# Kernel tuning notes

Measured on AMD Instinct MI355X. Metric: run time of the kernel, lower is better.

## Reference

```python
import jax, jax.numpy as jnp
import numpy as np

EPS = 1e-5
C = 512


def conv1x1(x, w, b):
    # 1x1 conv == per-pixel linear: x [B,C,H,W], w [O,C], b [O]
    return jnp.einsum('bchw,oc->bohw', x, w) + b[None, :, None, None]


def mean_variance_norm(feat):
    # per (batch, channel) normalization over spatial dims, unbiased var + eps
    b, c, h, w = feat.shape
    flat = feat.reshape(b, c, h * w)
    mean = flat.mean(axis=2)[:, :, None, None]
    std = jnp.sqrt(jnp.var(flat, axis=2, ddof=1) + EPS)[:, :, None, None]
    return (feat - mean) / std


def setup_inputs() -> dict:
    key = jax.random.key(0)
    ks = jax.random.split(key, 10)
    sc = 1.0 / np.sqrt(C)
    inp = {
        'content': jax.random.normal(ks[0], (2, C, 64, 64), jnp.float32),
        'style': jax.random.normal(ks[1], (2, C, 64, 64), jnp.float32),
        'f_w': jax.random.normal(ks[2], (C, C), jnp.float32) * sc,
        'f_b': jnp.zeros((C,), jnp.float32),
        'g_w': jax.random.normal(ks[3], (C, C), jnp.float32) * sc,
        'g_b': jnp.zeros((C,), jnp.float32),
        'h_w': jax.random.normal(ks[4], (C, C), jnp.float32) * sc,
        'h_b': jnp.zeros((C,), jnp.float32),
        'out_w': jax.random.normal(ks[5], (C, C), jnp.float32) * sc,
        'out_b': jnp.zeros((C,), jnp.float32),
    }
    return inp


def reference(content, style, f_w, f_b, g_w, g_b, h_w, h_b, out_w, out_b):
    b, c, h, w = content.shape
    Fq = conv1x1(content, f_w, f_b).reshape(b, c, h * w).transpose(0, 2, 1)  # [b,Nc,C]
    Gk = conv1x1(style, g_w, g_b).reshape(b, c, -1)                           # [b,C,Ns]
    Hv = conv1x1(style, h_w, h_b).reshape(b, c, -1).transpose(0, 2, 1)        # [b,Ns,C]

    S = jax.nn.softmax(jnp.einsum('bnc,bcs->bns', Fq, Gk), axis=-1)           # [b,Nc,Ns]
    mean = jnp.einsum('bns,bsc->bnc', S, Hv)                                   # E[x]
    second = jnp.einsum('bns,bsc->bnc', S, Hv * Hv)                            # E[x^2]
    std = jnp.sqrt(jnp.maximum(second - mean * mean, 0.0))

    mean = mean.reshape(b, h, w, c).transpose(0, 3, 1, 2)
    std = std.reshape(b, h, w, c).transpose(0, 3, 1, 2)

    O = std * mean_variance_norm(content) + mean
    O = conv1x1(O, out_w, out_b)
    return O + content
```

## Files before the change

### kernel.cpp

```cpp
#include <hip/hip_runtime.h>
#include <math.h>

#define NS 4096
#define CH 512
#define EPSV 1e-5f

typedef __attribute__((ext_vector_type(8))) _Float16 f16x8;
typedef __attribute__((ext_vector_type(4))) float f32x4;
typedef unsigned short u16;

__device__ __forceinline__ u16 f2h(float x) {
    _Float16 h = (_Float16)x;
    return __builtin_bit_cast(unsigned short, h);
}
__device__ __forceinline__ float h2f(u16 b) {
    return (float)__builtin_bit_cast(_Float16, b);
}

__device__ __forceinline__ void gload16(const void* g, void* l) {
    __builtin_amdgcn_global_load_lds((const __attribute__((address_space(1))) unsigned*)g,
                                     (__attribute__((address_space(3))) unsigned*)l, 16, 0, 0);
}

struct ZTab {
    long aoff[6];
    long boff[6];
    long ooff[6];
    long coff[6];
    int  mode[6];
    int  np[6];
    const float* bias[6];
};

template<int NPZ, bool GS>
__device__ __forceinline__ void kloop(
    const u16* __restrict__ pAhi, const u16* __restrict__ pAlo,
    const u16* __restrict__ pBhi,
    u16* smem, int smemStride,
    int Mw, int Nw, int K, int m0, int n0,
    int wid, int lane, int lk, int lm, int wm, int wn,
    const float* __restrict__ cbase,
    f32x4 (&acc)[4][4])
{
    auto stage = [&](int buf, int ks) {
        const int kp0 = ks << 2;
        #pragma unroll
        for (int i = 0; i < 2 * NPZ; ++i) {
            const int q = i * 4 + wid;
            const int b = q >> 3;
            const int p = (q & 7) >> 1;
            const int w = ((q & 1) << 6) + lane;
            const u16* src;
            if (b == 0)      src = pAhi + ((size_t)(kp0 + p) * Mw + m0 + w) * 8;
            else if (b == 1) src = pBhi + ((size_t)(kp0 + p) * Nw + n0 + w) * 8;
            else             src = pAlo + ((size_t)(kp0 + p) * Mw + m0 + w) * 8;
            gload16(src, &smem[(size_t)buf * smemStride + (size_t)(((b * 4 + p) * 128) + w) * 8]);
        }
    };

    const int nK = K >> 5;
    stage(0, 0);
    __syncthreads();
    int cur = 0;
    _Float16 ch[4] = {};
    for (int ks = 0; ks < nK; ++ks) {
        if (GS && (ks & 3) == 0) {
            const int g = ks >> 2;
            #pragma unroll
            for (int j = 0; j < 4; ++j)
                ch[j] = (_Float16)cbase[(size_t)g * NS + n0 + wn * 64 + j * 16 + lm];
        }
        if (ks + 1 < nK) stage(cur ^ 1, ks + 1);
        const u16* sm = smem + (size_t)cur * smemStride;
        f16x8 ah[4], bh[4], al[4];
        #pragma unroll
        for (int f = 0; f < 4; ++f) {
            ah[f] = *(const f16x8*)&sm[((0 * 4 + lk) * 128 + wm * 64 + f * 16 + lm) * 8];
            bh[f] = *(const f16x8*)&sm[((1 * 4 + lk) * 128 + wn * 64 + f * 16 + lm) * 8];
            if (GS) bh[f] = bh[f] * ch[f];
            if (NPZ == 3)
                al[f] = *(const f16x8*)&sm[((2 * 4 + lk) * 128 + wm * 64 + f * 16 + lm) * 8];
        }
        #pragma unroll
        for (int i = 0; i < 4; ++i)
            #pragma unroll
            for (int j = 0; j < 4; ++j) {
                acc[i][j] = __builtin_amdgcn_mfma_f32_16x16x32_f16(ah[i], bh[j], acc[i][j], 0, 0, 0);
                if (NPZ == 3)
                    acc[i][j] = __builtin_amdgcn_mfma_f32_16x16x32_f16(al[i], bh[j], acc[i][j], 0, 0, 0);
            }
        __syncthreads();
        cur ^= 1;
    }
}

template<int NP, bool RESID, bool COLST, bool GS>
__global__ __launch_bounds__(256, (NP == 2 ? 4 : 3)) void gemm_split(
    const u16* __restrict__ Ahi, const u16* __restrict__ Alo,
    const u16* __restrict__ Bhi,
    const float* __restrict__ resid,
    float* __restrict__ outF, u16* __restrict__ outH,
    float* __restrict__ pmg, float* __restrict__ psg,
    const float* __restrict__ cb,
    int Mw, int Nw, int K, ZTab tab)
{
    __shared__ u16 smem[2][NP * 4 * 128 * 8];
    const int t = threadIdx.x;
    const int lane = t & 63;
    const int wid = t >> 6;
    const int wm = wid >> 1, wn = wid & 1;
    const int lk = lane >> 4, lm = lane & 15;
    const int m0 = blockIdx.y * 128, n0 = blockIdx.x * 128;
    const int z = blockIdx.z;
    const int npz = tab.np[z];
    const u16* pAhi = Ahi + tab.aoff[z];
    const u16* pAlo = Alo + tab.aoff[z];
    const u16* pBhi = Bhi + tab.boff[z];
    const float* cbase = GS ? (cb + tab.coff[z]) : nullptr;

    f32x4 acc[4][4] = {};
    const int smemStride = NP * 4 * 128 * 8;

    if constexpr (NP == 2) {
        kloop<2, GS>(pAhi, pAlo, pBhi, &smem[0][0], smemStride,
                     Mw, Nw, K, m0, n0, wid, lane, lk, lm, wm, wn, cbase, acc);
    } else {
        if (npz == 2)
            kloop<2, GS>(pAhi, pAlo, pBhi, &smem[0][0], smemStride,
                         Mw, Nw, K, m0, n0, wid, lane, lk, lm, wm, wn, cbase, acc);
        else
            kloop<3, GS>(pAhi, pAlo, pBhi, &smem[0][0], smemStride,
                         Mw, Nw, K, m0, n0, wid, lane, lk, lm, wm, wn, cbase, acc);
    }

    const float* bp = tab.bias[z];
    if (COLST) {
        float* smx = (float*)&smem[0][0];
        float* ssm = smx + 256;
        #pragma unroll
        for (int j = 0; j < 4; ++j) {
            float mx = -3.0e38f;
            #pragma unroll
            for (int i = 0; i < 4; ++i)
                #pragma unroll
                for (int r = 0; r < 4; ++r)
                    mx = fmaxf(mx, acc[i][j][r]);
            mx = fmaxf(mx, __shfl_xor(mx, 16));
            mx = fmaxf(mx, __shfl_xor(mx, 32));
            float sum = 0.f;
            #pragma unroll
            for (int i = 0; i < 4; ++i)
                #pragma unroll
                for (int r = 0; r < 4; ++r)
                    sum += __expf(acc[i][j][r] - mx);
            sum += __shfl_xor(sum, 16);
            sum += __shfl_xor(sum, 32);
            if (lk == 0) {
                const int nloc = wn * 64 + j * 16 + lm;
                smx[wm * 128 + nloc] = mx;
                ssm[wm * 128 + nloc] = sum;
            }
        }
        __syncthreads();
        float mxc[4];
        #pragma unroll
        for (int j = 0; j < 4; ++j) {
            const int nloc = wn * 64 + j * 16 + lm;
            const float m0v = smx[nloc], m1v = smx[128 + nloc];
            const float mc = fmaxf(m0v, m1v);
            mxc[j] = mc;
            if (wm == 0 && lk == 0) {
                const float sc = ssm[nloc] * __expf(m0v - mc) + ssm[128 + nloc] * __expf(m1v - mc);
                const int n = n0 + nloc;
                const size_t gi = ((size_t)z * 32 + (m0 >> 7)) * NS + n;
                pmg[gi] = mc;
                psg[gi] = sc;
            }
        }
        u16* ph = outH + tab.ooff[z];
        #pragma unroll
        for (int i = 0; i < 4; ++i) {
            const long rg = (long)((m0 + wm * 64) >> 3) + i * 2 + (lk >> 1);
            const int sub = (lk & 1) * 4;
            #pragma unroll
            for (int j = 0; j < 4; ++j) {
                const int n = n0 + wn * 64 + j * 16 + lm;
                const long idx = (rg * Nw + n) * 8 + sub;
                u16 h[4];
                #pragma unroll
                for (int r = 0; r < 4; ++r)
                    h[r] = f2h(__expf(acc[i][j][r] - mxc[j]));
                *(ushort4*)&ph[idx] = make_ushort4(h[0], h[1], h[2], h[3]);
            }
        }
    } else if (tab.mode[z] == 0) {
        float* pout = outF + tab.ooff[z];
        #pragma unroll
        for (int i = 0; i < 4; ++i) {
            #pragma unroll
            for (int r = 0; r < 4; ++r) {
                const int m = m0 + wm * 64 + i * 16 + lk * 4 + r;
                const float bv = bp ? bp[m] : 0.f;
                const size_t ro = (size_t)m * Nw + n0 + wn * 64 + lm;
                #pragma unroll
                for (int j = 0; j < 4; ++j) {
                    float v = acc[i][j][r] + bv;
                    if (RESID) v += resid[tab.ooff[z] + ro + j * 16];
                    pout[ro + j * 16] = v;
                }
            }
        }
    } else {
        u16* ph = outH + tab.ooff[z];
        #pragma unroll
        for (int i = 0; i < 4; ++i) {
            float bv[4];
            #pragma unroll
            for (int r = 0; r < 4; ++r) {
                const int m = m0 + wm * 64 + i * 16 + lk * 4 + r;
                bv[r] = bp ? bp[m] : 0.f;
            }
            const long rg = (long)((m0 + wm * 64) >> 3) + i * 2 + (lk >> 1);
            const int sub = (lk & 1) * 4;
            #pragma unroll
            for (int j = 0; j < 4; ++j) {
                const int n = n0 + wn * 64 + j * 16 + lm;
                const long idx = (rg * Nw + n) * 8 + sub;
                u16 h[4];
                #pragma unroll
                for (int r = 0; r < 4; ++r)
                    h[r] = f2h(acc[i][j][r] + bv[r]);
                *(ushort4*)&ph[idx] = make_ushort4(h[0], h[1], h[2], h[3]);
            }
        }
    }
}

__global__ __launch_bounds__(256) void packB_k(const float* __restrict__ X,
    u16* __restrict__ Hi, int Nw, long xB, long pB)
{
    const int n = blockIdx.x * 256 + threadIdx.x;
    const int p = blockIdx.y;
    const int z = blockIdx.z;
    const float* Xp = X + (size_t)z * xB + ((size_t)p * 8) * Nw + n;
    u16 hi[8];
    #pragma unroll
    for (int j = 0; j < 8; ++j)
        hi[j] = f2h(Xp[(size_t)j * Nw]);
    const size_t o = (size_t)z * pB + ((size_t)p * Nw + n) * 8;
    *(uint4*)&Hi[o] = *(const uint4*)hi;
}

__global__ __launch_bounds__(256) void packA_T(const float* __restrict__ W,
    u16* __restrict__ Hi, int Kdim)
{
    __shared__ float tile[64][65];
    const int t = threadIdx.x;
    const int k0 = blockIdx.x * 64, m0 = blockIdx.y * 64;
    const int kk = t & 63, mb = t >> 6;
    #pragma unroll
    for (int it = 0; it < 16; ++it) {
        int mm = mb + it * 4;
        tile[mm][kk] = W[(size_t)(m0 + mm) * Kdim + k0 + kk];
    }
    __syncthreads();
    #pragma unroll
    for (int cc = 0; cc < 2; ++cc) {
        int c = t + cc * 256;
        int kp = c >> 6, m = c & 63;
        u16 hi[8];
        #pragma unroll
        for (int j = 0; j < 8; ++j)
            hi[j] = f2h(tile[m][kp * 8 + j]);
        size_t o = ((size_t)(k0 / 8 + kp) * CH + m0 + m) * 8;
        *(uint4*)&Hi[o] = *(const uint4*)hi;
    }
}

__global__ __launch_bounds__(256) void pack_hvT(const float* __restrict__ Hv,
    u16* __restrict__ H1h, u16* __restrict__ H2h, u16* __restrict__ H2l)
{
    __shared__ float tile[64][65];
    const int t = threadIdx.x;
    const int s0 = blockIdx.x * 64, c0 = blockIdx.y * 64;
    const int z = blockIdx.z;
    const float* src = Hv + (size_t)z * CH * NS;
    const int ss = t & 63, cb = t >> 6;
    #pragma unroll
    for (int it = 0; it < 16; ++it) {
        int cc = cb + it * 4;
        tile[cc][ss] = src[(size_t)(c0 + cc) * NS + s0 + ss];
    }
    __syncthreads();
    const size_t zb = (size_t)z * NS * CH;
    #pragma unroll
    for (int cc2 = 0; cc2 < 2; ++cc2) {
        int c = t + cc2 * 256;
        int sp = c >> 6, cm = c & 63;
        u16 h1[8], h2[8], l2[8];
        #pragma unroll
        for (int j = 0; j < 8; ++j) {
            float v = tile[cm][sp * 8 + j];
            u16 a = f2h(v);
            h1[j] = a;
            float q = h2f(a);
            float q2 = q * q;
            u16 b = f2h(q2);
            h2[j] = b;
            l2[j] = f2h(q2 - h2f(b));
        }
        size_t o = zb + ((size_t)(s0 / 8 + sp) * CH + c0 + cm) * 8;
        *(uint4*)&H1h[o] = *(const uint4*)h1;
        *(uint4*)&H2h[o] = *(const uint4*)h2;
        *(uint4*)&H2l[o] = *(const uint4*)l2;
    }
}

__global__ __launch_bounds__(256) void colstats_comb32(const float* __restrict__ pm,
    const float* __restrict__ ps, float* __restrict__ mx, float* __restrict__ inv)
{
    const int n = blockIdx.x * 256 + threadIdx.x;
    const int z = blockIdx.y;
    float m = -3.0e38f, s = 0.f;
    #pragma unroll 8
    for (int g = 0; g < 32; ++g) {
        float gm = pm[((size_t)z * 32 + g) * NS + n], gs = ps[((size_t)z * 32 + g) * NS + n];
        float nm = fmaxf(m, gm);
        s = s * __expf(m - nm) + gs * __expf(gm - nm);
        m = nm;
    }
    mx[(size_t)z * NS + n] = m;
    inv[(size_t)z * NS + n] = 1.f / s;
}

__global__ __launch_bounds__(256) void scale_c(const float* __restrict__ pm,
    const float* __restrict__ mxv, const float* __restrict__ invv,
    float* __restrict__ c)
{
    const int n = blockIdx.x * 256 + threadIdx.x;
    const int g = blockIdx.y;
    const int z = blockIdx.z;
    const size_t gi = ((size_t)z * 32 + g) * NS + n;
    c[gi] = __expf(pm[gi] - mxv[(size_t)z * NS + n]) * invv[(size_t)z * NS + n];
}

__global__ __launch_bounds__(256) void content_stats(const float* __restrict__ content,
                                                     float* __restrict__ cmean,
                                                     float* __restrict__ cinv)
{
    const int bc = blockIdx.x;
    const float4* p = (const float4*)(content + (size_t)bc * NS);
    const int t = threadIdx.x;
    float s = 0.f, s2 = 0.f;
    #pragma unroll
    for (int j = 0; j < 4; ++j) {
        float4 v = p[t + j * 256];
        s  += (v.x + v.y) + (v.z + v.w);
        s2 += (v.x * v.x + v.y * v.y) + (v.z * v.z + v.w * v.w);
    }
    #pragma unroll
    for (int off = 32; off >= 1; off >>= 1) {
        s  += __shfl_xor(s, off);
        s2 += __shfl_xor(s2, off);
    }
    __shared__ float r1[4], r2[4];
    const int wid = t >> 6;
    if ((t & 63) == 0) { r1[wid] = s; r2[wid] = s2; }
    __syncthreads();
    if (t == 0) {
        s  = (r1[0] + r1[1]) + (r1[2] + r1[3]);
        s2 = (r2[0] + r2[1]) + (r2[2] + r2[3]);
        const float mean = s * (1.0f / 4096.f);
        const float var = (s2 - 4096.f * mean * mean) * (1.0f / 4095.f);
        cmean[bc] = mean;
        cinv[bc] = rsqrtf(fmaxf(var, 0.f) + EPSV);
    }
}

__global__ __launch_bounds__(256) void compute_O_pack(
    const float* __restrict__ Mean, const float* __restrict__ Sec,
    const float* __restrict__ content,
    const float* __restrict__ cmean, const float* __restrict__ cinv,
    u16* __restrict__ Oh)
{
    const int n  = blockIdx.x * 256 + threadIdx.x;
    const int cg = blockIdx.y;
    const int b  = blockIdx.z;
    const size_t KN = (size_t)CH * NS;
    u16 h[8];
    #pragma unroll
    for (int j = 0; j < 8; ++j) {
        const int c = cg * 8 + j;
        const size_t po = (size_t)b * KN + (size_t)c * NS + n;
        const float mn = Mean[po];
        const float sc = Sec[po];
        const float ct = content[po];
        const int bc = b * CH + c;
        const float o = sqrtf(fmaxf(sc - mn * mn, 0.f)) * ((ct - cmean[bc]) * cinv[bc]) + mn;
        h[j] = f2h(o);
    }
    const size_t off = (size_t)b * KN + ((size_t)cg * NS + n) * 8;
    *(uint4*)&Oh[off] = *(const uint4*)h;
}

extern "C" void kernel_launch(void* const* d_in, const int* in_sizes, int n_in,
                              void* d_out, int out_size, void* d_ws, size_t ws_size,
                              hipStream_t stream)
{
    const float* content = (const float*)d_in[0];
    const float* style   = (const float*)d_in[1];
    const float* f_w   = (const float*)d_in[2];
    const float* f_b   = (const float*)d_in[3];
    const float* g_w   = (const float*)d_in[4];
    const float* g_b   = (const float*)d_in[5];
    const float* h_w   = (const float*)d_in[6];
    const float* h_b   = (const float*)d_in[7];
    const float* out_w = (const float*)d_in[8];
    const float* out_b = (const float*)d_in[9];
    float* out = (float*)d_out;

    char* ws = (char*)d_ws;
    size_t off = 0;
    auto alloc = [&](size_t bytes) -> void* {
        void* p = ws + off;
        off = (off + bytes + 255) & ~(size_t)255;
        return p;
    };

    const size_t KN   = (size_t)CH * NS;
    const size_t CHCH = (size_t)CH * CH;
    const long   NSNS = (long)NS * NS;

    u16* Wh0 = (u16*)alloc(4 * CHCH * 2);
    u16* Whv[4] = { Wh0, Wh0 + CHCH, Wh0 + 2 * CHCH, Wh0 + 3 * CHCH };

    u16* R2 = (u16*)alloc(6 * KN * 2);
    u16* Xc_hi = R2;
    u16* Xs_hi = R2 + 2 * KN;
    u16* HvT_hi  = R2;
    u16* Hv2T_hi = R2 + 2 * KN;
    u16* Hv2T_lo = R2 + 4 * KN;

    u16* Fqp_hi = (u16*)alloc(2 * KN * 2);
    u16* Gkp_hi = (u16*)alloc(2 * KN * 2);
    u16* Op_hi  = Gkp_hi;

    char* R5 = (char*)alloc(2 * (size_t)NS * NS * 2);
    float* Hv32 = (float*)(R5 + 4 * KN * 4);
    u16*   E16  = (u16*)R5;

    float* Mean32 = (float*)alloc(2 * KN * 4);
    float* Sec32  = (float*)alloc(2 * KN * 4);

    float* pm    = (float*)alloc(2 * 32 * NS * 4);
    float* ps    = (float*)alloc(2 * 32 * NS * 4);
    float* mxv   = (float*)alloc(2 * NS * 4);
    float* invv  = (float*)alloc(2 * NS * 4);
    float* ctab  = (float*)alloc(2 * 32 * NS * 4);
    float* cmean = (float*)alloc(1024 * 4);
    float* cinv  = (float*)alloc(1024 * 4);
    (void)ws_size; (void)in_sizes; (void)n_in; (void)out_size;

    packA_T<<<dim3(8, 8), 256, 0, stream>>>(f_w,   Whv[0], CH);
    packA_T<<<dim3(8, 8), 256, 0, stream>>>(g_w,   Whv[1], CH);
    packA_T<<<dim3(8, 8), 256, 0, stream>>>(h_w,   Whv[2], CH);
    packA_T<<<dim3(8, 8), 256, 0, stream>>>(out_w, Whv[3], CH);
    packB_k<<<dim3(16, 64, 2), 256, 0, stream>>>(content, Xc_hi, NS, (long)KN, (long)KN);
    packB_k<<<dim3(16, 64, 2), 256, 0, stream>>>(style,   Xs_hi, NS, (long)KN, (long)KN);
    content_stats<<<1024, 256, 0, stream>>>(content, cmean, cinv);

    {
        ZTab tb = {};
        const float* bs[3] = { f_b, g_b, h_b };
        for (int z = 0; z < 6; ++z) {
            const int w = z >> 1, b = z & 1;
            tb.aoff[z] = (long)w * CHCH;
            tb.boff[z] = (w == 0 ? 0 : (long)(2 * KN)) + (long)b * KN;
            tb.mode[z] = (w < 2) ? 1 : 0;
            tb.np[z]   = 2;
            tb.ooff[z] = (w < 2) ? ((long)w * 2 * KN + (long)b * KN)
                                 : ((long)4 * KN + (long)b * KN);
            tb.bias[z] = bs[w];
        }
        gemm_split<2, false, false, false><<<dim3(32, 4, 6), 256, 0, stream>>>(
            Wh0, nullptr, Xc_hi, nullptr,
            (float*)R5, Fqp_hi, nullptr, nullptr, nullptr, CH, NS, CH, tb);
    }

    pack_hvT<<<dim3(64, 8, 2), 256, 0, stream>>>(Hv32, HvT_hi, Hv2T_hi, Hv2T_lo);

    {
        ZTab tq = {};
        for (int z = 0; z < 2; ++z) {
            tq.aoff[z] = (long)z * KN;
            tq.boff[z] = (long)z * KN;
            tq.ooff[z] = (long)z * NSNS;
            tq.np[z]   = 2;
        }
        gemm_split<2, false, true, false><<<dim3(32, 32, 2), 256, 0, stream>>>(
            Gkp_hi, nullptr, Fqp_hi, nullptr,
            nullptr, E16, pm, ps, nullptr, NS, NS, CH, tq);
    }
    colstats_comb32<<<dim3(16, 2), 256, 0, stream>>>(pm, ps, mxv, invv);
    scale_c<<<dim3(16, 32, 2), 256, 0, stream>>>(pm, mxv, invv, ctab);

    {
        ZTab tp = {};
        for (int z = 0; z < 4; ++z) {
            const int sec = (z >> 1), b = z & 1;
            tp.aoff[z] = (long)sec * 2 * KN + (long)b * KN;
            tp.boff[z] = (long)b * NSNS;
            tp.ooff[z] = (long)sec * 2 * KN + (long)b * KN;
            tp.coff[z] = (long)b * 32 * NS;
            tp.np[z]   = sec ? 3 : 2;
        }
        gemm_split<3, false, false, true><<<dim3(32, 4, 4), 256, 0, stream>>>(
            R2, R2 + 2 * KN, E16, nullptr,
            Mean32, nullptr, nullptr, nullptr, ctab, CH, NS, NS, tp);
    }

    compute_O_pack<<<dim3(16, 64, 2), 256, 0, stream>>>(
        Mean32, Sec32, content, cmean, cinv, Op_hi);

    {
        ZTab tf = {};
        for (int z = 0; z < 2; ++z) {
            tf.ooff[z] = (long)z * KN;
            tf.boff[z] = (long)z * KN;
            tf.np[z]   = 2;
            tf.bias[z] = out_b;
        }
        gemm_split<2, true, false, false><<<dim3(32, 4, 2), 256, 0, stream>>>(
            Whv[3], nullptr, Op_hi, content,
            out, nullptr, nullptr, nullptr, nullptr, CH, NS, CH, tf);
    }
}
```

Baseline: 245.6 us.

## Split-K the attention-value GEMM and merge small pack/softmax-scale launches

```diff
diff --git a/kernel.cpp b/kernel.cpp
--- a/kernel.cpp
+++ b/kernel.cpp
@@ -23,14 +23,17 @@
 }
 
 struct ZTab {
-    long aoff[6];
-    long boff[6];
-    long ooff[6];
-    long coff[6];
-    int  mode[6];
-    int  np[6];
-    const float* bias[6];
+    long aoff[8];
+    long boff[8];
+    long ooff[8];
+    long coff[8];
+    int  mode[8];
+    int  np[8];
+    const float* bias[8];
 };
+
+struct PA4 { const float* w[4]; };
+struct PB2 { const float* x[2]; };
 
 template<int NPZ, bool GS>
 __device__ __forceinline__ void kloop(
@@ -236,32 +239,33 @@
     }
 }
 
-__global__ __launch_bounds__(256) void packB_k(const float* __restrict__ X,
-    u16* __restrict__ Hi, int Nw, long xB, long pB)
+__global__ __launch_bounds__(256) void packB4(PB2 xs, u16* __restrict__ Hi)
 {
     const int n = blockIdx.x * 256 + threadIdx.x;
     const int p = blockIdx.y;
     const int z = blockIdx.z;
-    const float* Xp = X + (size_t)z * xB + ((size_t)p * 8) * Nw + n;
+    const size_t KN = (size_t)CH * NS;
+    const float* Xp = xs.x[z >> 1] + (size_t)(z & 1) * KN + ((size_t)p * 8) * NS + n;
     u16 hi[8];
     #pragma unroll
     for (int j = 0; j < 8; ++j)
-        hi[j] = f2h(Xp[(size_t)j * Nw]);
-    const size_t o = (size_t)z * pB + ((size_t)p * Nw + n) * 8;
+        hi[j] = f2h(Xp[(size_t)j * NS]);
+    const size_t o = (size_t)z * KN + ((size_t)p * NS + n) * 8;
     *(uint4*)&Hi[o] = *(const uint4*)hi;
 }
 
-__global__ __launch_bounds__(256) void packA_T(const float* __restrict__ W,
-    u16* __restrict__ Hi, int Kdim)
+__global__ __launch_bounds__(256) void packA4(PA4 ws, u16* __restrict__ Hi)
 {
     __shared__ float tile[64][65];
     const int t = threadIdx.x;
     const int k0 = blockIdx.x * 64, m0 = blockIdx.y * 64;
+    const float* W = ws.w[blockIdx.z];
+    u16* H = Hi + (size_t)blockIdx.z * CH * CH;
     const int kk = t & 63, mb = t >> 6;
     #pragma unroll
     for (int it = 0; it < 16; ++it) {
         int mm = mb + it * 4;
-        tile[mm][kk] = W[(size_t)(m0 + mm) * Kdim + k0 + kk];
+        tile[mm][kk] = W[(size_t)(m0 + mm) * CH + k0 + kk];
     }
     __syncthreads();
     #pragma unroll
@@ -273,7 +277,7 @@
         for (int j = 0; j < 8; ++j)
             hi[j] = f2h(tile[m][kp * 8 + j]);
         size_t o = ((size_t)(k0 / 8 + kp) * CH + m0 + m) * 8;
-        *(uint4*)&Hi[o] = *(const uint4*)hi;
+        *(uint4*)&H[o] = *(const uint4*)hi;
     }
 }
 
@@ -317,7 +321,7 @@
 }
 
 __global__ __launch_bounds__(256) void colstats_comb32(const float* __restrict__ pm,
-    const float* __restrict__ ps, float* __restrict__ mx, float* __restrict__ inv)
+    const float* __restrict__ ps, float* __restrict__ ctab)
 {
     const int n = blockIdx.x * 256 + threadIdx.x;
     const int z = blockIdx.y;
@@ -329,19 +333,12 @@
         s = s * __expf(m - nm) + gs * __expf(gm - nm);
         m = nm;
     }
-    mx[(size_t)z * NS + n] = m;
-    inv[(size_t)z * NS + n] = 1.f / s;
-}
-
-__global__ __launch_bounds__(256) void scale_c(const float* __restrict__ pm,
-    const float* __restrict__ mxv, const float* __restrict__ invv,
-    float* __restrict__ c)
-{
-    const int n = blockIdx.x * 256 + threadIdx.x;
-    const int g = blockIdx.y;
-    const int z = blockIdx.z;
-    const size_t gi = ((size_t)z * 32 + g) * NS + n;
-    c[gi] = __expf(pm[gi] - mxv[(size_t)z * NS + n]) * invv[(size_t)z * NS + n];
+    const float inv = 1.f / s;
+    #pragma unroll 8
+    for (int g = 0; g < 32; ++g) {
+        const size_t gi = ((size_t)z * 32 + g) * NS + n;
+        ctab[gi] = __expf(pm[gi] - m) * inv;
+    }
 }
 
 __global__ __launch_bounds__(256) void content_stats(const float* __restrict__ content,
@@ -378,7 +375,7 @@
 }
 
 __global__ __launch_bounds__(256) void compute_O_pack(
-    const float* __restrict__ Mean, const float* __restrict__ Sec,
+    const float* __restrict__ MS,
     const float* __restrict__ content,
     const float* __restrict__ cmean, const float* __restrict__ cinv,
     u16* __restrict__ Oh)
@@ -392,8 +389,8 @@
     for (int j = 0; j < 8; ++j) {
         const int c = cg * 8 + j;
         const size_t po = (size_t)b * KN + (size_t)c * NS + n;
-        const float mn = Mean[po];
-        const float sc = Sec[po];
+        const float mn = MS[po] + MS[po + 4 * KN];
+        const float sc = MS[po + 2 * KN] + MS[po + 6 * KN];
         const float ct = content[po];
         const int bc = b * CH + c;
         const float o = sqrtf(fmaxf(sc - mn * mn, 0.f)) * ((ct - cmean[bc]) * cinv[bc]) + mn;
@@ -432,14 +429,13 @@
     const long   NSNS = (long)NS * NS;
 
     u16* Wh0 = (u16*)alloc(4 * CHCH * 2);
-    u16* Whv[4] = { Wh0, Wh0 + CHCH, Wh0 + 2 * CHCH, Wh0 + 3 * CHCH };
 
     u16* R2 = (u16*)alloc(6 * KN * 2);
     u16* Xc_hi = R2;
-    u16* Xs_hi = R2 + 2 * KN;
     u16* HvT_hi  = R2;
     u16* Hv2T_hi = R2 + 2 * KN;
     u16* Hv2T_lo = R2 + 4 * KN;
+    (void)HvT_hi;
 
     u16* Fqp_hi = (u16*)alloc(2 * KN * 2);
     u16* Gkp_hi = (u16*)alloc(2 * KN * 2);
@@ -449,24 +445,21 @@
     float* Hv32 = (float*)(R5 + 4 * KN * 4);
     u16*   E16  = (u16*)R5;
 
-    float* Mean32 = (float*)alloc(2 * KN * 4);
-    float* Sec32  = (float*)alloc(2 * KN * 4);
+    float* MS = (float*)alloc(8 * KN * 4);
 
     float* pm    = (float*)alloc(2 * 32 * NS * 4);
     float* ps    = (float*)alloc(2 * 32 * NS * 4);
-    float* mxv   = (float*)alloc(2 * NS * 4);
-    float* invv  = (float*)alloc(2 * NS * 4);
     float* ctab  = (float*)alloc(2 * 32 * NS * 4);
     float* cmean = (float*)alloc(1024 * 4);
     float* cinv  = (float*)alloc(1024 * 4);
     (void)ws_size; (void)in_sizes; (void)n_in; (void)out_size;
 
-    packA_T<<<dim3(8, 8), 256, 0, stream>>>(f_w,   Whv[0], CH);
-    packA_T<<<dim3(8, 8), 256, 0, stream>>>(g_w,   Whv[1], CH);
-    packA_T<<<dim3(8, 8), 256, 0, stream>>>(h_w,   Whv[2], CH);
-    packA_T<<<dim3(8, 8), 256, 0, stream>>>(out_w, Whv[3], CH);
-    packB_k<<<dim3(16, 64, 2), 256, 0, stream>>>(content, Xc_hi, NS, (long)KN, (long)KN);
-    packB_k<<<dim3(16, 64, 2), 256, 0, stream>>>(style,   Xs_hi, NS, (long)KN, (long)KN);
+    {
+        PA4 pa = { { f_w, g_w, h_w, out_w } };
+        packA4<<<dim3(8, 8, 4), 256, 0, stream>>>(pa, Wh0);
+        PB2 pb = { { content, style } };
+        packB4<<<dim3(16, 64, 4), 256, 0, stream>>>(pb, Xc_hi);
+    }
     content_stats<<<1024, 256, 0, stream>>>(content, cmean, cinv);
 
     {
@@ -487,7 +480,7 @@
             (float*)R5, Fqp_hi, nullptr, nullptr, nullptr, CH, NS, CH, tb);
     }
 
-    pack_hvT<<<dim3(64, 8, 2), 256, 0, stream>>>(Hv32, HvT_hi, Hv2T_hi, Hv2T_lo);
+    pack_hvT<<<dim3(64, 8, 2), 256, 0, stream>>>(Hv32, R2, Hv2T_hi, Hv2T_lo);
 
     {
         ZTab tq = {};
@@ -501,37 +494,37 @@
             Gkp_hi, nullptr, Fqp_hi, nullptr,
             nullptr, E16, pm, ps, nullptr, NS, NS, CH, tq);
     }
-    colstats_comb32<<<dim3(16, 2), 256, 0, stream>>>(pm, ps, mxv, invv);
-    scale_c<<<dim3(16, 32, 2), 256, 0, stream>>>(pm, mxv, invv, ctab);
+    colstats_comb32<<<dim3(16, 2), 256, 0, stream>>>(pm, ps, ctab);
 
     {
         ZTab tp = {};
-        for (int z = 0; z < 4; ++z) {
-            const int sec = (z >> 1), b = z & 1;
-            tp.aoff[z] = (long)sec * 2 * KN + (long)b * KN;
-            tp.boff[z] = (long)b * NSNS;
-            tp.ooff[z] = (long)sec * 2 * KN + (long)b * KN;
-            tp.coff[z] = (long)b * 32 * NS;
+        for (int z = 0; z < 8; ++z) {
+            const int p = z >> 2, sec = (z >> 1) & 1, b = z & 1;
+            tp.aoff[z] = (long)sec * 2 * KN + (long)b * KN + (long)p * (KN / 2);
+            tp.boff[z] = (long)b * NSNS + (long)p * (NSNS / 2);
+            tp.ooff[z] = (long)p * 4 * KN + (long)sec * 2 * KN + (long)b * KN;
+            tp.coff[z] = (long)b * 32 * NS + (long)p * 16 * NS;
             tp.np[z]   = sec ? 3 : 2;
         }
-        gemm_split<3, false, false, true><<<dim3(32, 4, 4), 256, 0, stream>>>(
+        gemm_split<3, false, false, true><<<dim3(32, 4, 8), 256, 0, stream>>>(
             R2, R2 + 2 * KN, E16, nullptr,
-            Mean32, nullptr, nullptr, nullptr, ctab, CH, NS, NS, tp);
+            MS, nullptr, nullptr, nullptr, ctab, CH, NS, NS / 2, tp);
     }
 
     compute_O_pack<<<dim3(16, 64, 2), 256, 0, stream>>>(
-        Mean32, Sec32, content, cmean, cinv, Op_hi);
+        MS, content, cmean, cinv, Op_hi);
 
     {
         ZTab tf = {};
         for (int z = 0; z < 2; ++z) {
+            tf.aoff[z] = (long)3 * CHCH;
             tf.ooff[z] = (long)z * KN;
             tf.boff[z] = (long)z * KN;
             tf.np[z]   = 2;
             tf.bias[z] = out_b;
         }
         gemm_split<2, true, false, false><<<dim3(32, 4, 2), 256, 0, stream>>>(
-            Whv[3], nullptr, Op_hi, content,
+            Wh0, nullptr, Op_hi, content,
             out, nullptr, nullptr, nullptr, nullptr, CH, NS, CH, tf);
     }
 }
```

After: 234.4 us. 4.5% less time.
